# Performance work log

Hardware: AMD Instinct MI355X
Metric: run time of the kernel (lower is better)

The kernel has to match this reference:

```python
import jax, jax.numpy as jnp
import numpy as np

D_MODEL = 1024
NUM_HEADS = 16
HEAD_DIM = D_MODEL // NUM_HEADS
B, N = 4, 2048


def setup_inputs() -> dict:
    key = jax.random.key(0)
    ks = jax.random.split(key, 9)
    s = 1.0 / np.sqrt(D_MODEL)
    inp = {
        "x": jax.random.normal(ks[0], (B, N, D_MODEL), dtype=jnp.float32),
        "Wq": jax.random.normal(ks[1], (D_MODEL, D_MODEL), dtype=jnp.float32) * s,
        "bq": jnp.zeros((D_MODEL,), dtype=jnp.float32),
        "Wk": jax.random.normal(ks[2], (D_MODEL, D_MODEL), dtype=jnp.float32) * s,
        "bk": jnp.zeros((D_MODEL,), dtype=jnp.float32),
        "Wv": jax.random.normal(ks[3], (D_MODEL, D_MODEL), dtype=jnp.float32) * s,
        "bv": jnp.zeros((D_MODEL,), dtype=jnp.float32),
        "Wo": jax.random.normal(ks[4], (D_MODEL, D_MODEL), dtype=jnp.float32) * s,
        "bo": jnp.zeros((D_MODEL,), dtype=jnp.float32),
    }
    return inp


def reference(x, Wq, bq, Wk, bk, Wv, bv, Wo, bo):
    b, n, c = x.shape
    h, d = NUM_HEADS, HEAD_DIM
    # QKV projections -> [B, H, N, d]
    q = (x @ Wq + bq).reshape(b, n, h, d).transpose(0, 2, 1, 3)
    k = (x @ Wk + bk).reshape(b, n, h, d).transpose(0, 2, 1, 3)
    v = (x @ Wv + bv).reshape(b, n, h, d).transpose(0, 2, 1, 3)
    scores = jnp.einsum("bhqd,bhkd->bhqk", q, k) / np.sqrt(d).astype(jnp.float32)
    attn = jax.nn.softmax(scores, axis=-1)  # dropout p=0 -> identity
    out = jnp.einsum("bhqk,bhkd->bhqd", attn, v)
    out = out.transpose(0, 2, 1, 3).reshape(b, n, c)
    return out @ Wo + bo
```

## Files before the change

### kernel.cpp

```cpp
#include <hip/hip_runtime.h>
#include <hip/hip_bf16.h>
#include <stdint.h>

#define DM 1024
#define SEQL 2048
#define NBATCH 4
#define NHEAD 16
#define HDIM 64
#define MTOT (NBATCH * SEQL)

using f32x4 = __attribute__((ext_vector_type(4))) float;
using f32x16 = __attribute__((ext_vector_type(16))) float;
using bf16x8 = __attribute__((ext_vector_type(8))) short;

static __device__ __forceinline__ unsigned short f2bf(float f) {
  union { float f; uint32_t u; } v; v.f = f;
  uint32_t u = v.u;
  return (unsigned short)((u + 0x7FFFu + ((u >> 16) & 1u)) >> 16);
}

static __device__ __forceinline__ float exp2_fast(float x) {
#if __has_builtin(__builtin_amdgcn_exp2f)
  return __builtin_amdgcn_exp2f(x);
#else
  float r;
  asm("v_exp_f32 %0, %1" : "=v"(r) : "v"(x));
  return r;
#endif
}

static __device__ __forceinline__ uint32_t pkbf(float lo, float hi) {
  float2 f; f.x = lo; f.y = hi;
  __hip_bfloat162 h = __float22bfloat162_rn(f);
  union { __hip_bfloat162 h; uint32_t u; } cv; cv.h = h;
  return cv.u;
}

static __device__ __forceinline__ f32x16 zero16() {
  f32x16 z;
#pragma unroll
  for (int i = 0; i < 16; ++i) z[i] = 0.f;
  return z;
}

static __device__ __forceinline__ void gload16(const void* g, void* l) {
  __builtin_amdgcn_global_load_lds(
      (const __attribute__((address_space(1))) unsigned int*)g,
      (__attribute__((address_space(3))) unsigned int*)l,
      16, 0, 0);
}

__global__ __launch_bounds__(256) void transpose_convert4(
    const float* __restrict__ W0, const float* __restrict__ W1,
    const float* __restrict__ W2, const float* __restrict__ W3,
    unsigned short* __restrict__ T0, unsigned short* __restrict__ T1,
    unsigned short* __restrict__ T2, unsigned short* __restrict__ T3) {
  __shared__ float tile[64][65];
  const int z = blockIdx.z;
  const float* W = z == 0 ? W0 : z == 1 ? W1 : z == 2 ? W2 : W3;
  unsigned short* WT = z == 0 ? T0 : z == 1 ? T1 : z == 2 ? T2 : T3;
  const int bx = blockIdx.x;
  const int by = blockIdx.y;
  const int t = threadIdx.x;
  const int r = t >> 4;
  const int c4 = (t & 15) * 4;
#pragma unroll
  for (int i = 0; i < 4; ++i) {
    const float4 v = *reinterpret_cast<const float4*>(
        &W[(size_t)(by * 64 + r + i * 16) * DM + bx * 64 + c4]);
    tile[r + i * 16][c4 + 0] = v.x;
    tile[r + i * 16][c4 + 1] = v.y;
    tile[r + i * 16][c4 + 2] = v.z;
    tile[r + i * 16][c4 + 3] = v.w;
  }
  __syncthreads();
#pragma unroll
  for (int i = 0; i < 4; ++i) {
    const int rr = r + i * 16;
    uint32_t lo = (uint32_t)f2bf(tile[c4 + 0][rr]) | ((uint32_t)f2bf(tile[c4 + 1][rr]) << 16);
    uint32_t hi = (uint32_t)f2bf(tile[c4 + 2][rr]) | ((uint32_t)f2bf(tile[c4 + 3][rr]) << 16);
    uint2 o; o.x = lo; o.y = hi;
    *reinterpret_cast<uint2*>(&WT[(size_t)(bx * 64 + rr) * DM + by * 64 + c4]) = o;
  }
}

__global__ __launch_bounds__(256) void convert_x(
    const float* __restrict__ x, unsigned short* __restrict__ xb) {
  const int i = blockIdx.x * 256 + threadIdx.x;
  const float4 v = reinterpret_cast<const float4*>(x)[i];
  uint2 o;
  o.x = (uint32_t)f2bf(v.x) | ((uint32_t)f2bf(v.y) << 16);
  o.y = (uint32_t)f2bf(v.z) | ((uint32_t)f2bf(v.w) << 16);
  reinterpret_cast<uint2*>(xb)[i] = o;
}

#define QSCALE 0.1803368801111204f

template <int MODE, int NNT>
__global__ __launch_bounds__(512) void gemm_big(
    const unsigned short* __restrict__ A, const unsigned short* __restrict__ B,
    const float* __restrict__ bias0, const float* __restrict__ bias1,
    void* __restrict__ out0, void* __restrict__ out1) {
  __shared__ unsigned short Abuf[4][256 * 32];
  __shared__ unsigned short Bbuf[4][128 * 32];

  const int tid = threadIdx.x;
  const int w = tid >> 6;
  const int lane = tid & 63;

  const int cpx = gridDim.x >> 3;
  const int bid = (blockIdx.x & 7) * cpx + (blockIdx.x >> 3);
  const int m0 = (bid / NNT) * 256;
  const int n0 = (bid % NNT) * 128;

  const int srow = tid >> 2;
  const int scol = (((lane & 3) ^ ((lane >> 3) & 3))) << 3;
  unsigned short* ldsA0 = &Abuf[0][w * 512];
  unsigned short* ldsA1 = &Abuf[0][4096 + w * 512];
  unsigned short* ldsB  = &Bbuf[0][w * 512];

#define STAGE(tt, bb)                                                          \
  {                                                                            \
    const int kk = (tt) * 32;                                                  \
    gload16(&A[(size_t)(m0 + srow) * DM + kk + scol], ldsA0 + (bb) * 8192);    \
    gload16(&A[(size_t)(m0 + 128 + srow) * DM + kk + scol], ldsA1 + (bb) * 8192); \
    gload16(&B[(size_t)(n0 + srow) * DM + kk + scol], ldsB + (bb) * 4096);     \
  }

  const int wm = w >> 1;
  const int wn = w & 1;
  const int lrow = lane & 15;
  const int ls = lane >> 4;
  int aoff[4], boff[4];
#pragma unroll
  for (int m = 0; m < 4; ++m) {
    const int r = wm * 64 + m * 16 + lrow;
    aoff[m] = r * 32 + ((ls ^ ((r >> 1) & 3)) << 3);
  }
#pragma unroll
  for (int n = 0; n < 4; ++n) {
    const int r = wn * 64 + n * 16 + lrow;
    boff[n] = r * 32 + ((ls ^ ((r >> 1) & 3)) << 3);
  }

  f32x4 acc[4][4];
#pragma unroll
  for (int m = 0; m < 4; ++m)
#pragma unroll
    for (int n = 0; n < 4; ++n) acc[m][n] = (f32x4){0.f, 0.f, 0.f, 0.f};

  STAGE(0, 0);
  STAGE(1, 1);
  asm volatile("s_waitcnt vmcnt(3)" ::: "memory");
  __builtin_amdgcn_s_barrier();

  const int NK = DM / 32;
  for (int t = 0; t < NK; ++t) {
    const int b = t & 3;
    if (t + 2 < NK) STAGE(t + 2, (t + 2) & 3);

    bf16x8 af[4], bfr[4];
#pragma unroll
    for (int m = 0; m < 4; ++m)
      af[m] = *reinterpret_cast<const bf16x8*>(&Abuf[b][aoff[m]]);
#pragma unroll
    for (int n = 0; n < 4; ++n)
      bfr[n] = *reinterpret_cast<const bf16x8*>(&Bbuf[b][boff[n]]);

    __builtin_amdgcn_s_setprio(1);
#pragma unroll
    for (int m = 0; m < 4; ++m)
#pragma unroll
      for (int n = 0; n < 4; ++n)
        acc[m][n] = __builtin_amdgcn_mfma_f32_16x16x32_bf16(af[m], bfr[n], acc[m][n], 0, 0, 0);
    __builtin_amdgcn_s_setprio(0);

    asm volatile("s_waitcnt lgkmcnt(0)" ::: "memory");
    if (t < NK - 2) {
      asm volatile("s_waitcnt vmcnt(3)" ::: "memory");
    } else {
      asm volatile("s_waitcnt vmcnt(0)" ::: "memory");
    }
    __builtin_amdgcn_s_barrier();
  }
#undef STAGE

  if (MODE == 0) {
    const int isK = n0 >> 10;
    unsigned short* dst = isK ? (unsigned short*)out1 : (unsigned short*)out0;
    const float* bp = isK ? bias1 : bias0;
    const float sc = isK ? 1.f : QSCALE;
#pragma unroll
    for (int n = 0; n < 4; ++n) {
      const int col = (n0 & 1023) + wn * 64 + n * 16 + lrow;
      const float bb = bp[col];
      const int hh = col >> 6, dd = col & 63;
#pragma unroll
      for (int m = 0; m < 4; ++m) {
        const int rowb = m0 + wm * 64 + m * 16 + ls * 4;
#pragma unroll
        for (int r = 0; r < 4; ++r) {
          const int mg = rowb + r;
          const int bidx = mg >> 11;
          const int nn = mg & 2047;
          dst[((size_t)(bidx * NHEAD + hh) * SEQL + nn) * HDIM + dd] =
              f2bf((acc[m][n][r] + bb) * sc);
        }
      }
    }
  } else if (MODE == 1) {
#pragma unroll
    for (int m = 0; m < 4; ++m) {
#pragma unroll
      for (int r = 0; r < 4; ++r) {
        const int ch = m0 + wm * 64 + m * 16 + ls * 4 + r;
        const float bb = bias0[ch];
        const int hh = ch >> 6, dd = ch & 63;
#pragma unroll
        for (int n = 0; n < 4; ++n) {
          const int sq = n0 + wn * 64 + n * 16 + lrow;
          const int bidx = sq >> 11;
          const int nn = sq & 2047;
          ((unsigned short*)out0)[((size_t)(bidx * NHEAD + hh) * HDIM + dd) * SEQL + nn] =
              f2bf(acc[m][n][r] + bb);
        }
      }
    }
  } else {
#pragma unroll
    for (int n = 0; n < 4; ++n) {
      const int col = n0 + wn * 64 + n * 16 + lrow;
      const float bb = bias0[col];
#pragma unroll
      for (int m = 0; m < 4; ++m) {
        const int rowb = m0 + wm * 64 + m * 16 + ls * 4;
#pragma unroll
        for (int r = 0; r < 4; ++r) {
          ((float*)out0)[(size_t)(rowb + r) * DM + col] = acc[m][n][r] + bb;
        }
      }
    }
  }
}

__global__ __launch_bounds__(512) void attn_kernel(
    const unsigned short* __restrict__ q, const unsigned short* __restrict__ k,
    const unsigned short* __restrict__ vt, unsigned short* __restrict__ attn_out) {
  __shared__ unsigned short Ks[2][64 * 64];
  __shared__ unsigned short Vs[2][64 * 64];

  const int bid = blockIdx.x;
  const int l0 = (bid & 7) * 64 + (bid >> 3);
  const int bh = l0 >> 3;
  const int qt = l0 & 7;
  const int b = bh >> 4, h = bh & 15;

  const int tid = threadIdx.x;
  const int w = tid >> 6;
  const int lane = tid & 63;
  const int qv = lane & 31;
  const int hi = lane >> 5;
  const int qg0 = qt * 256 + w * 32;

  const unsigned short* qptr = q + (size_t)bh * SEQL * HDIM;
  const unsigned short* kptr = k + (size_t)bh * SEQL * HDIM;
  const unsigned short* vptr = vt + (size_t)bh * HDIM * SEQL;

  bf16x8 qb[4];
#pragma unroll
  for (int kc = 0; kc < 4; ++kc)
    qb[kc] = *reinterpret_cast<const bf16x8*>(&qptr[(qg0 + qv) * HDIM + kc * 16 + hi * 8]);

  bf16x8 ones;
#pragma unroll
  for (int i = 0; i < 8; ++i) ones[i] = (short)0x3F80;

  f32x16 acc0 = zero16(), acc1 = zero16(), accL = zero16();

  const int x7 = qv & 7;
  int off[4];
#pragma unroll
  for (int i = 0; i < 4; ++i) off[i] = ((2 * i + hi) ^ x7) << 3;

  const int srow = tid >> 3;
  const int sslot = tid & 7;
  const int sdst = srow * 64 + ((sslot ^ (srow & 7)) << 3);

  uint4 rk, rv;
#define LOADT(t)                                                                    \
  {                                                                                 \
    rk = *reinterpret_cast<const uint4*>(&kptr[((t) * 64 + srow) * HDIM + sslot * 8]); \
    rv = *reinterpret_cast<const uint4*>(&vptr[srow * SEQL + (t) * 64 + sslot * 8]);   \
  }

  LOADT(0);
  const int NT = SEQL / 64;
  for (int t = 0; t < NT; ++t) {
    const int c = t & 1;
    *reinterpret_cast<uint4*>(&Ks[c][sdst]) = rk;
    *reinterpret_cast<uint4*>(&Vs[c][sdst]) = rv;
    __syncthreads();
    if (t + 1 < NT) LOADT(t + 1);

    f32x16 p0 = zero16(), p1 = zero16();
    __builtin_amdgcn_s_setprio(1);
#pragma unroll
    for (int kc = 0; kc < 4; ++kc) {
      bf16x8 ka0 = *reinterpret_cast<const bf16x8*>(&Ks[c][qv * 64 + off[kc]]);
      bf16x8 ka1 = *reinterpret_cast<const bf16x8*>(&Ks[c][(32 + qv) * 64 + off[kc]]);
      p0 = __builtin_amdgcn_mfma_f32_32x32x16_bf16(ka0, qb[kc], p0, 0, 0, 0);
      p1 = __builtin_amdgcn_mfma_f32_32x32x16_bf16(ka1, qb[kc], p1, 0, 0, 0);
    }
    __builtin_amdgcn_s_setprio(0);

#pragma unroll
    for (int i = 0; i < 16; ++i) {
      p0[i] = exp2_fast(p0[i]);
      p1[i] = exp2_fast(p1[i]);
    }

    bf16x8 pa[4];
#pragma unroll
    for (int ks = 0; ks < 4; ++ks) {
      const int o = 8 * (ks & 1);
      uint32_t X1, X2, Y1, Y2;
      if (ks < 2) {
        X1 = pkbf(p0[o + 0], p0[o + 1]); X2 = pkbf(p0[o + 2], p0[o + 3]);
        Y1 = pkbf(p0[o + 4], p0[o + 5]); Y2 = pkbf(p0[o + 6], p0[o + 7]);
      } else {
        X1 = pkbf(p1[o + 0], p1[o + 1]); X2 = pkbf(p1[o + 2], p1[o + 3]);
        Y1 = pkbf(p1[o + 4], p1[o + 5]); Y2 = pkbf(p1[o + 6], p1[o + 7]);
      }
      asm("v_permlane32_swap_b32 %0, %1" : "+v"(X1), "+v"(Y1));
      asm("v_permlane32_swap_b32 %0, %1" : "+v"(X2), "+v"(Y2));
      union { uint32_t u[4]; bf16x8 v; } uu;
      uu.u[0] = X1; uu.u[1] = X2; uu.u[2] = Y1; uu.u[3] = Y2;
      pa[ks] = uu.v;
    }

    __builtin_amdgcn_s_setprio(1);
#pragma unroll
    for (int ks = 0; ks < 4; ++ks) {
      bf16x8 vb0 = *reinterpret_cast<const bf16x8*>(&Vs[c][qv * 64 + off[ks]]);
      bf16x8 vb1 = *reinterpret_cast<const bf16x8*>(&Vs[c][(32 + qv) * 64 + off[ks]]);
      acc0 = __builtin_amdgcn_mfma_f32_32x32x16_bf16(pa[ks], vb0, acc0, 0, 0, 0);
      acc1 = __builtin_amdgcn_mfma_f32_32x32x16_bf16(pa[ks], vb1, acc1, 0, 0, 0);
      accL = __builtin_amdgcn_mfma_f32_32x32x16_bf16(pa[ks], ones, accL, 0, 0, 0);
    }
    __builtin_amdgcn_s_setprio(0);
  }
#undef LOADT

#pragma unroll
  for (int rg = 0; rg < 16; ++rg) {
    const int crow = (rg & 3) + 8 * (rg >> 2) + 4 * hi;
    const float invl = 1.f / accL[rg];
    const int qg = qg0 + crow;
    const size_t base = ((size_t)(b * SEQL + qg) * NHEAD + h) * HDIM + qv;
    attn_out[base] = f2bf(acc0[rg] * invl);
    attn_out[base + 32] = f2bf(acc1[rg] * invl);
  }
}

extern "C" void kernel_launch(void* const* d_in, const int* in_sizes, int n_in,
                              void* d_out, int out_size, void* d_ws, size_t ws_size,
                              hipStream_t stream) {
  const float* x  = (const float*)d_in[0];
  const float* Wq = (const float*)d_in[1];
  const float* bq = (const float*)d_in[2];
  const float* Wk = (const float*)d_in[3];
  const float* bk = (const float*)d_in[4];
  const float* Wv = (const float*)d_in[5];
  const float* bv = (const float*)d_in[6];
  const float* Wo = (const float*)d_in[7];
  const float* bo = (const float*)d_in[8];

  char* ws = (char*)d_ws;
  unsigned short* wqT = (unsigned short*)(ws);
  unsigned short* wkT = wqT + 1024 * 1024;
  unsigned short* wvT = wkT + 1024 * 1024;
  unsigned short* woT = wvT + 1024 * 1024;
  unsigned short* xb   = (unsigned short*)(ws + (size_t)(8 << 20));
  unsigned short* attn = xb;
  unsigned short* qw   = (unsigned short*)(ws + (size_t)(24 << 20));
  unsigned short* kw   = (unsigned short*)(ws + (size_t)(40 << 20));
  unsigned short* vtw  = (unsigned short*)(ws + (size_t)(56 << 20));

  transpose_convert4<<<dim3(16, 16, 4), 256, 0, stream>>>(Wq, Wk, Wv, Wo, wqT, wkT, wvT, woT);
  convert_x<<<MTOT * DM / 4 / 256, 256, 0, stream>>>(x, xb);

  gemm_big<0, 16><<<512, 512, 0, stream>>>(xb, wqT, bq, bk, qw, kw);
  gemm_big<1, 64><<<256, 512, 0, stream>>>(wvT, xb, bv, nullptr, vtw, nullptr);

  attn_kernel<<<512, 512, 0, stream>>>(qw, kw, vtw, attn);

  gemm_big<2, 8><<<256, 512, 0, stream>>>(attn, woT, bo, nullptr, (float*)d_out, nullptr);
}
```

Before: 225.2 us.

## Fuse Q/K/V projections into one 256x256-tile GEMM with in-kernel V transpose

Replaces the 256x128-tile GEMM with a 256x256 tile and a BK=64 double buffer, and fuses the V projection into the same launch as Q/K. The V tiles get their transposed layout by swapping the MFMA operand order. The aim is fewer launches and more reuse per loaded byte. In exchange it uses larger LDS (128KB) and 128 accumulator registers. The pipeline also becomes shallower (2 stages with a full vmcnt(0) wait each iteration), and the output projection now runs only 128 blocks, which may underfill the CUs.

```diff
diff --git a/kernel.cpp b/kernel.cpp
--- a/kernel.cpp
+++ b/kernel.cpp
@@ -96,99 +96,115 @@
 
 #define QSCALE 0.1803368801111204f
 
-template <int MODE, int NNT>
-__global__ __launch_bounds__(512) void gemm_big(
+template <int MODE>
+__global__ __launch_bounds__(512, 2) void gemm_v2(
     const unsigned short* __restrict__ A, const unsigned short* __restrict__ B,
-    const float* __restrict__ bias0, const float* __restrict__ bias1,
-    void* __restrict__ out0, void* __restrict__ out1) {
-  __shared__ unsigned short Abuf[4][256 * 32];
-  __shared__ unsigned short Bbuf[4][128 * 32];
+    const float* __restrict__ bq, const float* __restrict__ bk, const float* __restrict__ bv,
+    void* __restrict__ out_q, void* __restrict__ out_k, void* __restrict__ out_v) {
+  constexpr int NNT = (MODE == 0) ? 12 : 4;
+  __shared__ unsigned short Abuf[2][256 * 64];
+  __shared__ unsigned short Bbuf[2][256 * 64];
 
   const int tid = threadIdx.x;
   const int w = tid >> 6;
   const int lane = tid & 63;
+  const int lrow = lane & 15;
+  const int lhi = lane >> 4;
+  const int wm = w >> 2;
+  const int wn = w & 3;
 
   const int cpx = gridDim.x >> 3;
   const int bid = (blockIdx.x & 7) * cpx + (blockIdx.x >> 3);
   const int m0 = (bid / NNT) * 256;
-  const int n0 = (bid % NNT) * 128;
-
-  const int srow = tid >> 2;
-  const int scol = (((lane & 3) ^ ((lane >> 3) & 3))) << 3;
-  unsigned short* ldsA0 = &Abuf[0][w * 512];
-  unsigned short* ldsA1 = &Abuf[0][4096 + w * 512];
-  unsigned short* ldsB  = &Bbuf[0][w * 512];
-
-#define STAGE(tt, bb)                                                          \
-  {                                                                            \
-    const int kk = (tt) * 32;                                                  \
-    gload16(&A[(size_t)(m0 + srow) * DM + kk + scol], ldsA0 + (bb) * 8192);    \
-    gload16(&A[(size_t)(m0 + 128 + srow) * DM + kk + scol], ldsA1 + (bb) * 8192); \
-    gload16(&B[(size_t)(n0 + srow) * DM + kk + scol], ldsB + (bb) * 4096);     \
-  }
-
-  const int wm = w >> 1;
-  const int wn = w & 1;
-  const int lrow = lane & 15;
-  const int ls = lane >> 4;
-  int aoff[4], boff[4];
-#pragma unroll
-  for (int m = 0; m < 4; ++m) {
-    const int r = wm * 64 + m * 16 + lrow;
-    aoff[m] = r * 32 + ((ls ^ ((r >> 1) & 3)) << 3);
-  }
-#pragma unroll
-  for (int n = 0; n < 4; ++n) {
-    const int r = wn * 64 + n * 16 + lrow;
-    boff[n] = r * 32 + ((ls ^ ((r >> 1) & 3)) << 3);
-  }
-
-  f32x4 acc[4][4];
-#pragma unroll
-  for (int m = 0; m < 4; ++m)
+  const int n0 = (bid % NNT) * 256;
+
+  const int srow = w * 8 + (lane >> 3);
+  const int sck = (lane & 7) ^ ((lane >> 3) & 7);
+
+#define STAGE(tt, bb)                                                           \
+  {                                                                             \
+    const int kk = (tt) * 64;                                                   \
+    _Pragma("unroll") for (int rr = 0; rr < 4; ++rr) {                          \
+      gload16(&A[(size_t)(m0 + rr * 64 + srow) * DM + kk + sck * 8],            \
+              (char*)&Abuf[bb][0] + (rr * 64 + w * 8) * 128);                   \
+      gload16(&B[(size_t)(n0 + rr * 64 + srow) * DM + kk + sck * 8],            \
+              (char*)&Bbuf[bb][0] + (rr * 64 + w * 8) * 128);                   \
+    }                                                                           \
+  }
+
+  const bool vswap = (MODE == 0) && (n0 >= 2048);
+
+  f32x4 acc[8][4];
+#pragma unroll
+  for (int m = 0; m < 8; ++m)
 #pragma unroll
     for (int n = 0; n < 4; ++n) acc[m][n] = (f32x4){0.f, 0.f, 0.f, 0.f};
 
   STAGE(0, 0);
-  STAGE(1, 1);
-  asm volatile("s_waitcnt vmcnt(3)" ::: "memory");
+  asm volatile("s_waitcnt vmcnt(0)" ::: "memory");
   __builtin_amdgcn_s_barrier();
 
-  const int NK = DM / 32;
+  const int NK = DM / 64;
   for (int t = 0; t < NK; ++t) {
-    const int b = t & 3;
-    if (t + 2 < NK) STAGE(t + 2, (t + 2) & 3);
-
-    bf16x8 af[4], bfr[4];
-#pragma unroll
-    for (int m = 0; m < 4; ++m)
-      af[m] = *reinterpret_cast<const bf16x8*>(&Abuf[b][aoff[m]]);
-#pragma unroll
-    for (int n = 0; n < 4; ++n)
-      bfr[n] = *reinterpret_cast<const bf16x8*>(&Bbuf[b][boff[n]]);
-
-    __builtin_amdgcn_s_setprio(1);
-#pragma unroll
-    for (int m = 0; m < 4; ++m)
-#pragma unroll
-      for (int n = 0; n < 4; ++n)
-        acc[m][n] = __builtin_amdgcn_mfma_f32_16x16x32_bf16(af[m], bfr[n], acc[m][n], 0, 0, 0);
-    __builtin_amdgcn_s_setprio(0);
+    const int b = t & 1;
+    if (t + 1 < NK) STAGE(t + 1, b ^ 1);
+
+#pragma unroll
+    for (int ks = 0; ks < 2; ++ks) {
+      bf16x8 af[8], bfr[4];
+#pragma unroll
+      for (int m = 0; m < 8; ++m) {
+        const int r = wm * 128 + m * 16 + lrow;
+        af[m] = *reinterpret_cast<const bf16x8*>(
+            &Abuf[b][r * 64 + (((ks * 4 + lhi) ^ (lane & 7)) << 3)]);
+      }
+#pragma unroll
+      for (int n = 0; n < 4; ++n) {
+        const int r = wn * 64 + n * 16 + lrow;
+        bfr[n] = *reinterpret_cast<const bf16x8*>(
+            &Bbuf[b][r * 64 + (((ks * 4 + lhi) ^ (lane & 7)) << 3)]);
+      }
+      __builtin_amdgcn_s_setprio(1);
+      if (vswap) {
+#pragma unroll
+        for (int m = 0; m < 8; ++m)
+#pragma unroll
+          for (int n = 0; n < 4; ++n)
+            acc[m][n] = __builtin_amdgcn_mfma_f32_16x16x32_bf16(bfr[n], af[m], acc[m][n], 0, 0, 0);
+      } else {
+#pragma unroll
+        for (int m = 0; m < 8; ++m)
+#pragma unroll
+          for (int n = 0; n < 4; ++n)
+            acc[m][n] = __builtin_amdgcn_mfma_f32_16x16x32_bf16(af[m], bfr[n], acc[m][n], 0, 0, 0);
+      }
+      __builtin_amdgcn_s_setprio(0);
+    }
 
     asm volatile("s_waitcnt lgkmcnt(0)" ::: "memory");
-    if (t < NK - 2) {
-      asm volatile("s_waitcnt vmcnt(3)" ::: "memory");
-    } else {
-      asm volatile("s_waitcnt vmcnt(0)" ::: "memory");
-    }
+    asm volatile("s_waitcnt vmcnt(0)" ::: "memory");
     __builtin_amdgcn_s_barrier();
   }
 #undef STAGE
 
-  if (MODE == 0) {
+  if (MODE == 1) {
+    float* Cout = (float*)out_q;
+#pragma unroll
+    for (int n = 0; n < 4; ++n) {
+      const int col = n0 + wn * 64 + n * 16 + lrow;
+      const float bb = bq[col];
+#pragma unroll
+      for (int m = 0; m < 8; ++m) {
+        const int rowb = m0 + wm * 128 + m * 16 + lhi * 4;
+#pragma unroll
+        for (int r = 0; r < 4; ++r)
+          Cout[(size_t)(rowb + r) * DM + col] = acc[m][n][r] + bb;
+      }
+    }
+  } else if (!vswap) {
     const int isK = n0 >> 10;
-    unsigned short* dst = isK ? (unsigned short*)out1 : (unsigned short*)out0;
-    const float* bp = isK ? bias1 : bias0;
+    unsigned short* dst = isK ? (unsigned short*)out_k : (unsigned short*)out_q;
+    const float* bp = isK ? bk : bq;
     const float sc = isK ? 1.f : QSCALE;
 #pragma unroll
     for (int n = 0; n < 4; ++n) {
@@ -196,8 +212,8 @@
       const float bb = bp[col];
       const int hh = col >> 6, dd = col & 63;
 #pragma unroll
-      for (int m = 0; m < 4; ++m) {
-        const int rowb = m0 + wm * 64 + m * 16 + ls * 4;
+      for (int m = 0; m < 8; ++m) {
+        const int rowb = m0 + wm * 128 + m * 16 + lhi * 4;
 #pragma unroll
         for (int r = 0; r < 4; ++r) {
           const int mg = rowb + r;
@@ -208,35 +224,22 @@
         }
       }
     }
-  } else if (MODE == 1) {
-#pragma unroll
-    for (int m = 0; m < 4; ++m) {
+  } else {
+    unsigned short* vo = (unsigned short*)out_v;
+#pragma unroll
+    for (int n = 0; n < 4; ++n) {
 #pragma unroll
       for (int r = 0; r < 4; ++r) {
-        const int ch = m0 + wm * 64 + m * 16 + ls * 4 + r;
-        const float bb = bias0[ch];
+        const int ch = (n0 - 2048) + wn * 64 + n * 16 + lhi * 4 + r;
+        const float bb = bv[ch];
         const int hh = ch >> 6, dd = ch & 63;
 #pragma unroll
-        for (int n = 0; n < 4; ++n) {
-          const int sq = n0 + wn * 64 + n * 16 + lrow;
-          const int bidx = sq >> 11;
-          const int nn = sq & 2047;
-          ((unsigned short*)out0)[((size_t)(bidx * NHEAD + hh) * HDIM + dd) * SEQL + nn] =
+        for (int m = 0; m < 8; ++m) {
+          const int seq = m0 + wm * 128 + m * 16 + lrow;
+          const int bidx = seq >> 11;
+          const int nn = seq & 2047;
+          vo[((size_t)(bidx * NHEAD + hh) * HDIM + dd) * SEQL + nn] =
               f2bf(acc[m][n][r] + bb);
-        }
-      }
-    }
-  } else {
-#pragma unroll
-    for (int n = 0; n < 4; ++n) {
-      const int col = n0 + wn * 64 + n * 16 + lrow;
-      const float bb = bias0[col];
-#pragma unroll
-      for (int m = 0; m < 4; ++m) {
-        const int rowb = m0 + wm * 64 + m * 16 + ls * 4;
-#pragma unroll
-        for (int r = 0; r < 4; ++r) {
-          ((float*)out0)[(size_t)(rowb + r) * DM + col] = acc[m][n][r] + bb;
         }
       }
     }
@@ -389,10 +392,10 @@
   transpose_convert4<<<dim3(16, 16, 4), 256, 0, stream>>>(Wq, Wk, Wv, Wo, wqT, wkT, wvT, woT);
   convert_x<<<MTOT * DM / 4 / 256, 256, 0, stream>>>(x, xb);
 
-  gemm_big<0, 16><<<512, 512, 0, stream>>>(xb, wqT, bq, bk, qw, kw);
-  gemm_big<1, 64><<<256, 512, 0, stream>>>(wvT, xb, bv, nullptr, vtw, nullptr);
+  gemm_v2<0><<<384, 512, 0, stream>>>(xb, wqT, bq, bk, bv, qw, kw, vtw);
 
   attn_kernel<<<512, 512, 0, stream>>>(qw, kw, vtw, attn);
 
-  gemm_big<2, 8><<<256, 512, 0, stream>>>(attn, woT, bo, nullptr, (float*)d_out, nullptr);
-}
+  gemm_v2<1><<<128, 512, 0, stream>>>(attn, woT, bo, nullptr, nullptr,
+                                      (float*)d_out, nullptr, nullptr);
+}
```

Measured after the change: 477.3 us. 112% more time.
